# Kernel tuning notes

Hardware: AMD Instinct MI355X
Metric: run time of the kernel (lower is better)

## Reference

```python
import jax, jax.numpy as jnp
import numpy as np

B, C_IN, N, HC = 32, 128, 8192, 64
HEAD_NAMES = ['hm', 'reg', 'height', 'dim', 'rot', 'iou']
HEAD_OUT = [3, 2, 1, 3, 2, 1]
EPS = 1e-5
INIT_BIAS = -2.19


def setup_inputs() -> dict:
    key = jax.random.key(0)
    ks = jax.random.split(key, 16)
    d = {}
    d['ct_feat'] = jax.random.normal(ks[0], (B, C_IN, N), jnp.float32)
    # shared conv (1x1) + BN1d params
    d['sh_w'] = jax.random.normal(ks[1], (HC, C_IN), jnp.float32) * 0.05
    d['sh_b'] = jnp.zeros((HC,), jnp.float32)
    d['sh_g'] = jnp.ones((HC,), jnp.float32)
    d['sh_beta'] = jnp.zeros((HC,), jnp.float32)
    d['sh_mean'] = jax.random.normal(ks[2], (HC,), jnp.float32) * 0.1
    d['sh_var'] = jax.random.uniform(ks[3], (HC,), jnp.float32) + 0.5
    # first conv layer of each SepHead branch (stacked over 6 heads)
    d['head_w1'] = jax.random.normal(ks[4], (6, HC, HC), jnp.float32) * 0.05
    d['head_b1'] = jnp.zeros((6, HC), jnp.float32)
    d['head_g1'] = jnp.ones((6, HC), jnp.float32)
    d['head_beta1'] = jnp.zeros((6, HC), jnp.float32)
    d['head_mean1'] = jax.random.normal(ks[5], (6, HC), jnp.float32) * 0.1
    d['head_var1'] = jax.random.uniform(ks[6], (6, HC), jnp.float32) + 0.5
    # final conv of each branch (distinct out channels)
    for i, (name, c_out) in enumerate(zip(HEAD_NAMES, HEAD_OUT)):
        d[name + '_w'] = jax.random.normal(ks[7 + i], (c_out, HC), jnp.float32) * 0.05
        if name == 'hm':  # hm final bias is filled with init_bias
            d[name + '_b'] = jnp.full((c_out,), INIT_BIAS, jnp.float32)
        else:
            d[name + '_b'] = jnp.zeros((c_out,), jnp.float32)
    return d


def _bn(x, g, b, m, v):
    # x: [B, C, N]; params: [C]
    return (x - m[:, None]) * jax.lax.rsqrt(v[:, None] + EPS) * g[:, None] + b[:, None]


def reference(ct_feat, sh_w, sh_b, sh_g, sh_beta, sh_mean, sh_var,
              head_w1, head_b1, head_g1, head_beta1, head_mean1, head_var1,
              hm_w, hm_b, reg_w, reg_b, height_w, height_b,
              dim_w, dim_b, rot_w, rot_b, iou_w, iou_b):
    # shared_conv: Conv1d(k=1) + BN1d + ReLU
    y = jnp.einsum('oc,bcn->bon', sh_w, ct_feat) + sh_b[:, None]
    y = jax.nn.relu(_bn(y, sh_g, sh_beta, sh_mean, sh_var))  # [B, HC, N]

    # first layer of all 6 head branches, batched over head axis h
    z = jnp.einsum('hoc,bcn->hbon', head_w1, y) + head_b1[:, None, :, None]
    z = (z - head_mean1[:, None, :, None]) * jax.lax.rsqrt(head_var1[:, None, :, None] + EPS)
    z = z * head_g1[:, None, :, None] + head_beta1[:, None, :, None]
    z = jax.nn.relu(z)  # [6, B, HC, N]

    finals = [(hm_w, hm_b), (reg_w, reg_b), (height_w, height_b),
              (dim_w, dim_b), (rot_w, rot_b), (iou_w, iou_b)]
    outs = [jnp.einsum('oc,bcn->bon', w, z[i]) + b[:, None]
            for i, (w, b) in enumerate(finals)]
    # concat in head order [hm(3), reg(2), height(1), dim(3), rot(2), iou(1)] -> [B, 12, N]
    return jnp.concatenate(outs, axis=1)
```

## Files before the change

kernel.cpp:

```cpp
#include <hip/hip_runtime.h>
#include <hip/hip_bf16.h>
#include <cstdint>

typedef __attribute__((ext_vector_type(8))) short bf16x8;
typedef __attribute__((ext_vector_type(4))) float f32x4;
typedef __attribute__((ext_vector_type(2))) int i32x2;

#define NCOL 8192

#define WS_AW 0
#define WS_A1 8192
#define WS_AF 32768
#define WS_U16_TOTAL 38912
#define WS_OFSH 19456
#define WS_OFH  19520
#define WS_BIAS 19904
#define PREP_TOTAL (WS_U16_TOTAL + 464)

union FragU { uint32_t u[4]; bf16x8 v; uint4 q; };

__device__ __forceinline__ uint16_t f2bf(float f) {
  uint32_t x = __builtin_bit_cast(uint32_t, f);
  x += 0x7fffu + ((x >> 16) & 1u);
  return (uint16_t)(x >> 16);
}
__device__ __forceinline__ uint32_t rne_bits(float f) {
  uint32_t x = __builtin_bit_cast(uint32_t, f);
  return x + 0x7fffu + ((x >> 16) & 1u);
}
__device__ __forceinline__ uint32_t pack_bf16(float lo, float hi) {
  return __builtin_amdgcn_perm(rne_bits(hi), rne_bits(lo), 0x07060302u);
}

__device__ __forceinline__ void cswap(uint32_t lo, uint32_t hi,
                                      uint32_t& f1, uint32_t& f2) {
  i32x2 t = __builtin_amdgcn_permlane32_swap((int)lo, (int)hi, false, false);
  i32x2 f = __builtin_amdgcn_permlane16_swap(t[0], t[1], false, false);
  f1 = (uint32_t)f[0];
  f2 = (uint32_t)f[1];
}

__global__ __launch_bounds__(256) void ch_prep(
    const float* __restrict__ shw, const float* __restrict__ shb,
    const float* __restrict__ shg, const float* __restrict__ shbeta,
    const float* __restrict__ shmean, const float* __restrict__ shvar,
    const float* __restrict__ w1, const float* __restrict__ b1,
    const float* __restrict__ g1, const float* __restrict__ beta1,
    const float* __restrict__ mean1, const float* __restrict__ var1,
    const float* __restrict__ hm_w, const float* __restrict__ hm_b,
    const float* __restrict__ reg_w, const float* __restrict__ reg_b,
    const float* __restrict__ height_w, const float* __restrict__ height_b,
    const float* __restrict__ dim_w, const float* __restrict__ dim_b,
    const float* __restrict__ rot_w, const float* __restrict__ rot_b,
    const float* __restrict__ iou_w, const float* __restrict__ iou_b,
    uint16_t* __restrict__ wsq)
{
  const int e = blockIdx.x * 256 + threadIdx.x;
  if (e >= PREP_TOTAL) return;
  const int rowbase[6] = {0, 3, 5, 6, 9, 11};
  const int couts[6]   = {3, 2, 1, 3, 2, 1};
  const float* wfp[6]  = {hm_w, reg_w, height_w, dim_w, rot_w, iou_w};

  if (e < WS_A1) {
    const int i = e & 7, q = (e >> 3) & 3, kc = (e >> 5) & 3, m = e >> 7;
    const int k = kc * 32 + q * 8 + i;
    const float sc = shg[m] * rsqrtf(shvar[m] + 1e-5f);
    wsq[e] = f2bf(shw[m * 128 + k] * sc);
  } else if (e < WS_AF) {
    const int e2 = e - WS_A1;
    const int i = e2 & 7, q = (e2 >> 3) & 3, kc = (e2 >> 5) & 1,
              m = (e2 >> 6) & 63, h = e2 >> 12;
    const int k = kc * 32 + q * 8 + i, row = h * 64 + m;
    const float sc = g1[row] * rsqrtf(var1[row] + 1e-5f);
    wsq[e] = f2bf(w1[row * 64 + k] * sc);
  } else if (e < WS_U16_TOTAL) {
    const int e2 = e - WS_AF;
    const int i = e2 & 7, q = (e2 >> 3) & 3, kc = (e2 >> 5) & 1,
              m = (e2 >> 6) & 15, h = e2 >> 10;
    const int k = kc * 32 + q * 8 + i, rr = m - rowbase[h];
    const float v = (rr >= 0 && rr < couts[h]) ? wfp[h][rr * 64 + k] : 0.f;
    wsq[e] = f2bf(v);
  } else {
    const int t2 = e - WS_U16_TOTAL;
    float* wff = (float*)wsq;
    float v = 0.f;
    if (t2 < 64) {
      const float sc = shg[t2] * rsqrtf(shvar[t2] + 1e-5f);
      v = (shb[t2] - shmean[t2]) * sc + shbeta[t2];
    } else if (t2 < 448) {
      const int i = t2 - 64;
      const float sc = g1[i] * rsqrtf(var1[i] + 1e-5f);
      v = (b1[i] - mean1[i]) * sc + beta1[i];
    } else {
      const int i = t2 - 448;
      if (i < 3)       v = hm_b[i];
      else if (i < 5)  v = reg_b[i - 3];
      else if (i < 6)  v = height_b[i - 5];
      else if (i < 9)  v = dim_b[i - 6];
      else if (i < 11) v = rot_b[i - 9];
      else if (i < 12) v = iou_b[i - 11];
    }
    wff[WS_OFSH + t2] = v;
  }
}

__global__ __launch_bounds__(256, 2) void ch_main(
    const float* __restrict__ ct,
    const uint16_t* __restrict__ wsq,
    const float* __restrict__ wsf,
    float* __restrict__ outp)
{
  __shared__ __align__(16) float sm_x[2][128 * 64];

  const int t    = threadIdx.x;
  const int wv   = t >> 6;
  const int lane = t & 63;
  const int l15  = lane & 15;
  const int qd   = lane >> 4;
  const int bid  = blockIdx.x;
  const int b    = bid >> 4;
  const int g    = bid & 15;
  const float* ctb = ct + (size_t)b * 128 * NCOL;

#define STAGE(bsel, it)                                                        \
  {                                                                            \
    const int col0_ = (g * 8 + (it)) * 64;                                     \
    _Pragma("unroll")                                                          \
    for (int i = 0; i < 8; ++i) {                                              \
      const int ii = wv * 8 + i;                                               \
      const int k  = 4 * ii + qd;                                              \
      const int sw = (k >> 3) & 3;                                             \
      const float* src = ctb + (size_t)k * NCOL + col0_ +                      \
                         ((4 * l15) ^ (sw << 4));                              \
      __builtin_amdgcn_global_load_lds(                                        \
          (const __attribute__((address_space(1))) uint32_t*)src,              \
          (__attribute__((address_space(3))) uint32_t*)&sm_x[bsel][ii * 256],  \
          16, 0, 0);                                                           \
    }                                                                          \
  }

  FragU aw[4][4];
  #pragma unroll
  for (int kc = 0; kc < 4; ++kc)
    #pragma unroll
    for (int mt = 0; mt < 4; ++mt)
      aw[kc][mt].q = *(const uint4*)(wsq + WS_AW + ((mt * 16 + l15) * 4 + kc) * 32 + qd * 8);
  f32x4 ofsh[4];
  #pragma unroll
  for (int mt = 0; mt < 4; ++mt)
    ofsh[mt] = *(const f32x4*)(wsf + WS_OFSH + mt * 16 + qd * 4);
  const f32x4 bs = *(const f32x4*)(wsf + WS_BIAS + (qd & 3) * 4);

  STAGE(0, 0);
  STAGE(1, 1);

  #pragma unroll 1
  for (int it = 0; it < 8; ++it) {
    const int bsel = it & 1;
    const int col0 = (g * 8 + it) * 64;

    if (it == 0)      asm volatile("s_waitcnt vmcnt(8)" ::: "memory");
    else if (it < 7)  asm volatile("s_waitcnt vmcnt(12)" ::: "memory");
    else              asm volatile("s_waitcnt vmcnt(0)" ::: "memory");
    __builtin_amdgcn_s_barrier();

    const float* smf = &sm_x[bsel][0];
    const int cx = (wv * 16 + l15) ^ (qd << 4);

    f32x4 accY[4];
    #pragma unroll
    for (int mt = 0; mt < 4; ++mt)
      accY[mt] = (f32x4){0.f, 0.f, 0.f, 0.f};

    #pragma unroll
    for (int kc = 0; kc < 4; ++kc) {
      FragU f;
      #pragma unroll
      for (int i2 = 0; i2 < 4; ++i2) {
        const int k = kc * 32 + qd * 8 + 2 * i2;
        const int w = k * 64 + cx;
        f.u[i2] = pack_bf16(smf[w], smf[w + 64]);
      }
      #pragma unroll
      for (int mt = 0; mt < 4; ++mt)
        accY[mt] = __builtin_amdgcn_mfma_f32_16x16x32_bf16(aw[kc][mt].v, f.v, accY[mt], 0, 0, 0);
    }
    __builtin_amdgcn_s_barrier();

    if (it < 6) STAGE(bsel, it + 2);

    FragU yfrag[2];
    {
      uint32_t P[4][2];
      #pragma unroll
      for (int mt = 0; mt < 4; ++mt) {
        const f32x4 v = accY[mt];
        P[mt][0] = pack_bf16(fmaxf(v[0] + ofsh[mt][0], 0.f), fmaxf(v[1] + ofsh[mt][1], 0.f));
        P[mt][1] = pack_bf16(fmaxf(v[2] + ofsh[mt][2], 0.f), fmaxf(v[3] + ofsh[mt][3], 0.f));
      }
      #pragma unroll
      for (int kc = 0; kc < 2; ++kc)
        #pragma unroll
        for (int u = 0; u < 2; ++u)
          cswap(P[2 * kc][u], P[2 * kc + 1][u], yfrag[kc].u[u], yfrag[kc].u[u + 2]);
    }

    f32x4 accO = (f32x4){0.f, 0.f, 0.f, 0.f};
    const uint16_t* a1p = wsq + WS_A1 + l15 * 64 + qd * 8;
    const uint16_t* afp = wsq + WS_AF + l15 * 64 + qd * 8;
    const float*    ofp = wsf + WS_OFH + qd * 4;

    #pragma unroll 1
    for (int h = 0; h < 6; ++h) {
      FragU wa[2][4];
      FragU af[2];
      f32x4 ofv[4];
      #pragma unroll
      for (int kc = 0; kc < 2; ++kc)
        #pragma unroll
        for (int mt = 0; mt < 4; ++mt)
          wa[kc][mt].q = *(const uint4*)(a1p + mt * 1024 + kc * 32);
      #pragma unroll
      for (int kc = 0; kc < 2; ++kc)
        af[kc].q = *(const uint4*)(afp + kc * 32);
      #pragma unroll
      for (int mt = 0; mt < 4; ++mt)
        ofv[mt] = *(const f32x4*)(ofp + mt * 16);

      f32x4 accZ[4];
      #pragma unroll
      for (int mt = 0; mt < 4; ++mt)
        accZ[mt] = (f32x4){0.f, 0.f, 0.f, 0.f};
      #pragma unroll
      for (int kc = 0; kc < 2; ++kc)
        #pragma unroll
        for (int mt = 0; mt < 4; ++mt)
          accZ[mt] = __builtin_amdgcn_mfma_f32_16x16x32_bf16(wa[kc][mt].v, yfrag[kc].v, accZ[mt], 0, 0, 0);

      uint32_t Q[4][2];
      #pragma unroll
      for (int mt = 0; mt < 4; ++mt) {
        const f32x4 v = accZ[mt];
        Q[mt][0] = pack_bf16(fmaxf(v[0] + ofv[mt][0], 0.f), fmaxf(v[1] + ofv[mt][1], 0.f));
        Q[mt][1] = pack_bf16(fmaxf(v[2] + ofv[mt][2], 0.f), fmaxf(v[3] + ofv[mt][3], 0.f));
      }
      FragU zf[2];
      #pragma unroll
      for (int kc = 0; kc < 2; ++kc)
        #pragma unroll
        for (int u = 0; u < 2; ++u)
          cswap(Q[2 * kc][u], Q[2 * kc + 1][u], zf[kc].u[u], zf[kc].u[u + 2]);
      #pragma unroll
      for (int kc = 0; kc < 2; ++kc)
        accO = __builtin_amdgcn_mfma_f32_16x16x32_bf16(af[kc].v, zf[kc].v, accO, 0, 0, 0);

      a1p += 4096;
      afp += 1024;
      ofp += 64;
    }

    if (qd < 3) {
      const int col = col0 + wv * 16 + l15;
      #pragma unroll
      for (int r = 0; r < 4; ++r)
        outp[((size_t)(b * 12 + qd * 4 + r)) * NCOL + col] = accO[r] + bs[r];
    }
  }
#undef STAGE
}

extern "C" void kernel_launch(void* const* d_in, const int* in_sizes, int n_in,
                              void* d_out, int out_size, void* d_ws, size_t ws_size,
                              hipStream_t stream) {
  (void)out_size; (void)ws_size;
  static const int sortedPos[25] = {
      0, 24, 19, 21, 20, 22, 23, 8, 3, 5, 4, 6, 7,
      12, 11, 16, 15, 10, 9, 2, 1, 18, 17, 14, 13};
  const bool sorted_order =
      (n_in == 25) && (in_sizes[1] == 3) && (in_sizes[2] == 192) &&
      (in_sizes[8] == 24576) && (in_sizes[24] == 8192);
  const float* p[25];
  for (int r = 0; r < 25; ++r)
    p[r] = (const float*)d_in[sorted_order ? sortedPos[r] : r];

  uint16_t* wsq = (uint16_t*)d_ws;

  hipLaunchKernelGGL(ch_prep, dim3((PREP_TOTAL + 255) / 256), dim3(256), 0, stream,
      p[1], p[2], p[3], p[4], p[5], p[6],
      p[7], p[8], p[9], p[10], p[11], p[12],
      p[13], p[14], p[15], p[16], p[17], p[18],
      p[19], p[20], p[21], p[22], p[23], p[24],
      wsq);

  hipLaunchKernelGGL(ch_main, dim3(512), dim3(256), 0, stream,
      p[0], (const uint16_t*)wsq, (const float*)wsq, (float*)d_out);
}
```

Measured before the change: 349.1 us.

## Replace persistent double-buffered tile loop with one tile per block

Each block now handles a single 64-column tile, and the grid grows from 512 to 4096 blocks. This removes the in-kernel double-buffered staging loop and its manual waitcnt schedule. Shared memory per block halves to 32 KB and the launch-bounds occupancy hint is dropped, so the hardware can keep more blocks resident and overlap loads across blocks rather than within one. The cost is reloading the shared weight fragments and offsets for every tile and losing explicit prefetch. A sched_barrier is also added after the per-head weight loads.

Measured after the change: 353.1 us. Within noise of the previous version (+1.1%).

```diff
diff --git a/kernel.cpp b/kernel.cpp
--- a/kernel.cpp
+++ b/kernel.cpp
@@ -104,13 +104,13 @@
   }
 }
 
-__global__ __launch_bounds__(256, 2) void ch_main(
+__global__ __launch_bounds__(256) void ch_main(
     const float* __restrict__ ct,
     const uint16_t* __restrict__ wsq,
     const float* __restrict__ wsf,
     float* __restrict__ outp)
 {
-  __shared__ __align__(16) float sm_x[2][128 * 64];
+  __shared__ __align__(16) float sm_x[128 * 64];
 
   const int t    = threadIdx.x;
   const int wv   = t >> 6;
@@ -118,25 +118,22 @@
   const int l15  = lane & 15;
   const int qd   = lane >> 4;
   const int bid  = blockIdx.x;
-  const int b    = bid >> 4;
-  const int g    = bid & 15;
+  const int b    = bid >> 7;
+  const int col0 = (bid & 127) * 64;
   const float* ctb = ct + (size_t)b * 128 * NCOL;
 
-#define STAGE(bsel, it)                                                        \
-  {                                                                            \
-    const int col0_ = (g * 8 + (it)) * 64;                                     \
-    _Pragma("unroll")                                                          \
-    for (int i = 0; i < 8; ++i) {                                              \
-      const int ii = wv * 8 + i;                                               \
-      const int k  = 4 * ii + qd;                                              \
-      const int sw = (k >> 3) & 3;                                             \
-      const float* src = ctb + (size_t)k * NCOL + col0_ +                      \
-                         ((4 * l15) ^ (sw << 4));                              \
-      __builtin_amdgcn_global_load_lds(                                        \
-          (const __attribute__((address_space(1))) uint32_t*)src,              \
-          (__attribute__((address_space(3))) uint32_t*)&sm_x[bsel][ii * 256],  \
-          16, 0, 0);                                                           \
-    }                                                                          \
+  {
+    #pragma unroll
+    for (int i = 0; i < 8; ++i) {
+      const int ii = wv * 8 + i;
+      const int k  = 4 * ii + qd;
+      const int sw = (k >> 3) & 3;
+      const float* src = ctb + (size_t)k * NCOL + col0 + ((4 * l15) ^ (sw << 4));
+      __builtin_amdgcn_global_load_lds(
+          (const __attribute__((address_space(1))) uint32_t*)src,
+          (__attribute__((address_space(3))) uint32_t*)&sm_x[ii * 256],
+          16, 0, 0);
+    }
   }
 
   FragU aw[4][4];
@@ -151,122 +148,107 @@
     ofsh[mt] = *(const f32x4*)(wsf + WS_OFSH + mt * 16 + qd * 4);
   const f32x4 bs = *(const f32x4*)(wsf + WS_BIAS + (qd & 3) * 4);
 
-  STAGE(0, 0);
-  STAGE(1, 1);
+  asm volatile("s_waitcnt vmcnt(0)" ::: "memory");
+  __builtin_amdgcn_s_barrier();
+
+  const int cx = (wv * 16 + l15) ^ (qd << 4);
+
+  f32x4 accY[4];
+  #pragma unroll
+  for (int mt = 0; mt < 4; ++mt)
+    accY[mt] = (f32x4){0.f, 0.f, 0.f, 0.f};
+
+  #pragma unroll
+  for (int kc = 0; kc < 4; ++kc) {
+    FragU f;
+    #pragma unroll
+    for (int i2 = 0; i2 < 4; ++i2) {
+      const int k = kc * 32 + qd * 8 + 2 * i2;
+      const int w = k * 64 + cx;
+      f.u[i2] = pack_bf16(sm_x[w], sm_x[w + 64]);
+    }
+    #pragma unroll
+    for (int mt = 0; mt < 4; ++mt)
+      accY[mt] = __builtin_amdgcn_mfma_f32_16x16x32_bf16(aw[kc][mt].v, f.v, accY[mt], 0, 0, 0);
+  }
+
+  FragU yfrag[2];
+  {
+    uint32_t P[4][2];
+    #pragma unroll
+    for (int mt = 0; mt < 4; ++mt) {
+      const f32x4 v = accY[mt];
+      P[mt][0] = pack_bf16(fmaxf(v[0] + ofsh[mt][0], 0.f), fmaxf(v[1] + ofsh[mt][1], 0.f));
+      P[mt][1] = pack_bf16(fmaxf(v[2] + ofsh[mt][2], 0.f), fmaxf(v[3] + ofsh[mt][3], 0.f));
+    }
+    #pragma unroll
+    for (int kc = 0; kc < 2; ++kc)
+      #pragma unroll
+      for (int u = 0; u < 2; ++u)
+        cswap(P[2 * kc][u], P[2 * kc + 1][u], yfrag[kc].u[u], yfrag[kc].u[u + 2]);
+  }
+
+  f32x4 accO = (f32x4){0.f, 0.f, 0.f, 0.f};
+  const uint16_t* a1p = wsq + WS_A1 + l15 * 64 + qd * 8;
+  const uint16_t* afp = wsq + WS_AF + l15 * 64 + qd * 8;
+  const float*    ofp = wsf + WS_OFH + qd * 4;
 
   #pragma unroll 1
-  for (int it = 0; it < 8; ++it) {
-    const int bsel = it & 1;
-    const int col0 = (g * 8 + it) * 64;
-
-    if (it == 0)      asm volatile("s_waitcnt vmcnt(8)" ::: "memory");
-    else if (it < 7)  asm volatile("s_waitcnt vmcnt(12)" ::: "memory");
-    else              asm volatile("s_waitcnt vmcnt(0)" ::: "memory");
-    __builtin_amdgcn_s_barrier();
-
-    const float* smf = &sm_x[bsel][0];
-    const int cx = (wv * 16 + l15) ^ (qd << 4);
-
-    f32x4 accY[4];
-    #pragma unroll
-    for (int mt = 0; mt < 4; ++mt)
-      accY[mt] = (f32x4){0.f, 0.f, 0.f, 0.f};
-
-    #pragma unroll
-    for (int kc = 0; kc < 4; ++kc) {
-      FragU f;
-      #pragma unroll
-      for (int i2 = 0; i2 < 4; ++i2) {
-        const int k = kc * 32 + qd * 8 + 2 * i2;
-        const int w = k * 64 + cx;
-        f.u[i2] = pack_bf16(smf[w], smf[w + 64]);
-      }
+  for (int h = 0; h < 6; ++h) {
+    FragU wa[2][4];
+    FragU af[2];
+    f32x4 ofv[4];
+    #pragma unroll
+    for (int kc = 0; kc < 2; ++kc)
       #pragma unroll
       for (int mt = 0; mt < 4; ++mt)
-        accY[mt] = __builtin_amdgcn_mfma_f32_16x16x32_bf16(aw[kc][mt].v, f.v, accY[mt], 0, 0, 0);
-    }
-    __builtin_amdgcn_s_barrier();
-
-    if (it < 6) STAGE(bsel, it + 2);
-
-    FragU yfrag[2];
-    {
-      uint32_t P[4][2];
-      #pragma unroll
-      for (int mt = 0; mt < 4; ++mt) {
-        const f32x4 v = accY[mt];
-        P[mt][0] = pack_bf16(fmaxf(v[0] + ofsh[mt][0], 0.f), fmaxf(v[1] + ofsh[mt][1], 0.f));
-        P[mt][1] = pack_bf16(fmaxf(v[2] + ofsh[mt][2], 0.f), fmaxf(v[3] + ofsh[mt][3], 0.f));
-      }
-      #pragma unroll
-      for (int kc = 0; kc < 2; ++kc)
-        #pragma unroll
-        for (int u = 0; u < 2; ++u)
-          cswap(P[2 * kc][u], P[2 * kc + 1][u], yfrag[kc].u[u], yfrag[kc].u[u + 2]);
-    }
-
-    f32x4 accO = (f32x4){0.f, 0.f, 0.f, 0.f};
-    const uint16_t* a1p = wsq + WS_A1 + l15 * 64 + qd * 8;
-    const uint16_t* afp = wsq + WS_AF + l15 * 64 + qd * 8;
-    const float*    ofp = wsf + WS_OFH + qd * 4;
-
-    #pragma unroll 1
-    for (int h = 0; h < 6; ++h) {
-      FragU wa[2][4];
-      FragU af[2];
-      f32x4 ofv[4];
-      #pragma unroll
-      for (int kc = 0; kc < 2; ++kc)
-        #pragma unroll
-        for (int mt = 0; mt < 4; ++mt)
-          wa[kc][mt].q = *(const uint4*)(a1p + mt * 1024 + kc * 32);
-      #pragma unroll
-      for (int kc = 0; kc < 2; ++kc)
-        af[kc].q = *(const uint4*)(afp + kc * 32);
+        wa[kc][mt].q = *(const uint4*)(a1p + mt * 1024 + kc * 32);
+    #pragma unroll
+    for (int kc = 0; kc < 2; ++kc)
+      af[kc].q = *(const uint4*)(afp + kc * 32);
+    #pragma unroll
+    for (int mt = 0; mt < 4; ++mt)
+      ofv[mt] = *(const f32x4*)(ofp + mt * 16);
+    __builtin_amdgcn_sched_barrier(0);
+
+    f32x4 accZ[4];
+    #pragma unroll
+    for (int mt = 0; mt < 4; ++mt)
+      accZ[mt] = (f32x4){0.f, 0.f, 0.f, 0.f};
+    #pragma unroll
+    for (int kc = 0; kc < 2; ++kc)
       #pragma unroll
       for (int mt = 0; mt < 4; ++mt)
-        ofv[mt] = *(const f32x4*)(ofp + mt * 16);
-
-      f32x4 accZ[4];
-      #pragma unroll
-      for (int mt = 0; mt < 4; ++mt)
-        accZ[mt] = (f32x4){0.f, 0.f, 0.f, 0.f};
-      #pragma unroll
-      for (int kc = 0; kc < 2; ++kc)
-        #pragma unroll
-        for (int mt = 0; mt < 4; ++mt)
-          accZ[mt] = __builtin_amdgcn_mfma_f32_16x16x32_bf16(wa[kc][mt].v, yfrag[kc].v, accZ[mt], 0, 0, 0);
-
-      uint32_t Q[4][2];
-      #pragma unroll
-      for (int mt = 0; mt < 4; ++mt) {
-        const f32x4 v = accZ[mt];
-        Q[mt][0] = pack_bf16(fmaxf(v[0] + ofv[mt][0], 0.f), fmaxf(v[1] + ofv[mt][1], 0.f));
-        Q[mt][1] = pack_bf16(fmaxf(v[2] + ofv[mt][2], 0.f), fmaxf(v[3] + ofv[mt][3], 0.f));
-      }
-      FragU zf[2];
-      #pragma unroll
-      for (int kc = 0; kc < 2; ++kc)
-        #pragma unroll
-        for (int u = 0; u < 2; ++u)
-          cswap(Q[2 * kc][u], Q[2 * kc + 1][u], zf[kc].u[u], zf[kc].u[u + 2]);
-      #pragma unroll
-      for (int kc = 0; kc < 2; ++kc)
-        accO = __builtin_amdgcn_mfma_f32_16x16x32_bf16(af[kc].v, zf[kc].v, accO, 0, 0, 0);
-
-      a1p += 4096;
-      afp += 1024;
-      ofp += 64;
-    }
-
-    if (qd < 3) {
-      const int col = col0 + wv * 16 + l15;
-      #pragma unroll
-      for (int r = 0; r < 4; ++r)
-        outp[((size_t)(b * 12 + qd * 4 + r)) * NCOL + col] = accO[r] + bs[r];
-    }
-  }
-#undef STAGE
+        accZ[mt] = __builtin_amdgcn_mfma_f32_16x16x32_bf16(wa[kc][mt].v, yfrag[kc].v, accZ[mt], 0, 0, 0);
+
+    uint32_t Q[4][2];
+    #pragma unroll
+    for (int mt = 0; mt < 4; ++mt) {
+      const f32x4 v = accZ[mt];
+      Q[mt][0] = pack_bf16(fmaxf(v[0] + ofv[mt][0], 0.f), fmaxf(v[1] + ofv[mt][1], 0.f));
+      Q[mt][1] = pack_bf16(fmaxf(v[2] + ofv[mt][2], 0.f), fmaxf(v[3] + ofv[mt][3], 0.f));
+    }
+    FragU zf[2];
+    #pragma unroll
+    for (int kc = 0; kc < 2; ++kc)
+      #pragma unroll
+      for (int u = 0; u < 2; ++u)
+        cswap(Q[2 * kc][u], Q[2 * kc + 1][u], zf[kc].u[u], zf[kc].u[u + 2]);
+    #pragma unroll
+    for (int kc = 0; kc < 2; ++kc)
+      accO = __builtin_amdgcn_mfma_f32_16x16x32_bf16(af[kc].v, zf[kc].v, accO, 0, 0, 0);
+
+    a1p += 4096;
+    afp += 1024;
+    ofp += 64;
+  }
+
+  if (qd < 3) {
+    const int col = col0 + wv * 16 + l15;
+    #pragma unroll
+    for (int r = 0; r < 4; ++r)
+      outp[((size_t)(b * 12 + qd * 4 + r)) * NCOL + col] = accO[r] + bs[r];
+  }
 }
 
 extern "C" void kernel_launch(void* const* d_in, const int* in_sizes, int n_in,
@@ -292,6 +274,6 @@
       p[19], p[20], p[21], p[22], p[23], p[24],
       wsq);
 
-  hipLaunchKernelGGL(ch_main, dim3(512), dim3(256), 0, stream,
+  hipLaunchKernelGGL(ch_main, dim3(4096), dim3(256), 0, stream,
       p[0], (const uint16_t*)wsq, (const float*)wsq, (float*)d_out);
 }
```
